# Kernel optimization log

Measured on AMD Instinct MI355X. Metric: run time of the kernel, lower is better.

The kernel has to match this reference:

```python
import jax, jax.numpy as jnp
import numpy as np

D_MODEL = 2048
NUM_Q_HEADS = 32
NUM_KV_HEADS = 8
HEAD_DIM = D_MODEL // NUM_Q_HEADS  # 64
NUM_GROUPS = NUM_Q_HEADS // NUM_KV_HEADS  # 4


def setup_inputs() -> dict:
    key = jax.random.key(0)
    ks = jax.random.split(key, 9)
    s = 1.0 / np.sqrt(D_MODEL)
    x = jax.random.normal(ks[0], (2, 2048, D_MODEL), dtype=jnp.float32)
    Wq = jax.random.uniform(ks[1], (D_MODEL, NUM_Q_HEADS * HEAD_DIM), jnp.float32, -s, s)
    bq = jax.random.uniform(ks[2], (NUM_Q_HEADS * HEAD_DIM,), jnp.float32, -s, s)
    Wk = jax.random.uniform(ks[3], (D_MODEL, NUM_KV_HEADS * HEAD_DIM), jnp.float32, -s, s)
    bk = jax.random.uniform(ks[4], (NUM_KV_HEADS * HEAD_DIM,), jnp.float32, -s, s)
    Wv = jax.random.uniform(ks[5], (D_MODEL, NUM_KV_HEADS * HEAD_DIM), jnp.float32, -s, s)
    bv = jax.random.uniform(ks[6], (NUM_KV_HEADS * HEAD_DIM,), jnp.float32, -s, s)
    Wo = jax.random.uniform(ks[7], (D_MODEL, D_MODEL), jnp.float32, -s, s)
    bo = jax.random.uniform(ks[8], (D_MODEL,), jnp.float32, -s, s)
    return {"x": x, "Wq": Wq, "bq": bq, "Wk": Wk, "bk": bk,
            "Wv": Wv, "bv": bv, "Wo": Wo, "bo": bo}


def reference(x, Wq, bq, Wk, bk, Wv, bv, Wo, bo):
    B, T, C = x.shape
    Hkv, G, Dh = NUM_KV_HEADS, NUM_GROUPS, HEAD_DIM
    # projections
    q = (x @ Wq + bq).reshape(B, T, Hkv, G, Dh)   # group G query heads per kv head
    k = (x @ Wk + bk).reshape(B, T, Hkv, Dh)
    v = (x @ Wv + bv).reshape(B, T, Hkv, Dh)
    scale = 1.0 / np.sqrt(Dh).astype(np.float32)
    # scores: [B, Hkv, G, T, T] (kv head broadcast over its G query heads)
    scores = jnp.einsum('btkgd,bskd->bkgts', q, k) * scale
    attn = jax.nn.softmax(scores, axis=-1)
    out = jnp.einsum('bkgts,bskd->btkgd', attn, v).reshape(B, T, C)
    return out @ Wo + bo
```

## Files before the change

kernel.cpp:

```cpp
#include <hip/hip_runtime.h>
#include <cstdint>
#include <cstddef>
#include <math.h>

typedef uint16_t bf16;
typedef __attribute__((ext_vector_type(8))) __bf16 bf16x8;
typedef __attribute__((ext_vector_type(4))) float f32x4;
typedef __attribute__((ext_vector_type(16))) float f32x16;

#define MFMA16(a,b,c) __builtin_amdgcn_mfma_f32_16x16x32_bf16((a),(b),(c),0,0,0)
#define MFMA32(a,b,c) __builtin_amdgcn_mfma_f32_32x32x16_bf16((a),(b),(c),0,0,0)

__device__ __forceinline__ uint16_t f2bf(float f){
  uint32_t u = __float_as_uint(f);
  return (uint16_t)((u + 0x7fffu + ((u >> 16) & 1u)) >> 16);
}
__device__ __forceinline__ uint32_t pk2(float lo, float hi){
  return (uint32_t)f2bf(lo) | ((uint32_t)f2bf(hi) << 16);
}

__device__ __forceinline__ void gload_lds16(const void* g, void* l){
  __builtin_amdgcn_global_load_lds((const __attribute__((address_space(1))) void*)g,
                                   (__attribute__((address_space(3))) void*)l, 16, 0, 0);
}

__device__ __forceinline__ void transpose64(const float* __restrict__ in, bf16* __restrict__ out,
                                            int R, int C, int c0, int r0, float* tileRaw){
  float (*tile)[65] = reinterpret_cast<float(*)[65]>(tileRaw);
  int t = threadIdx.x;
  int fx = t & 15, fy = t >> 4;
  #pragma unroll
  for (int i = 0; i < 4; i++){
    int r = fy + i*16;
    float4 v = *reinterpret_cast<const float4*>(in + (size_t)(r0 + r)*C + c0 + fx*4);
    tile[r][fx*4+0] = v.x; tile[r][fx*4+1] = v.y;
    tile[r][fx*4+2] = v.z; tile[r][fx*4+3] = v.w;
  }
  __syncthreads();
  int gx = t & 7, gy = t >> 3;
  #pragma unroll
  for (int i = 0; i < 2; i++){
    int c = gy + i*32;
    int rr = gx*8;
    union { bf16 h[8]; uint4 u; } pk_;
    #pragma unroll
    for (int j = 0; j < 8; j++) pk_.h[j] = f2bf(tile[rr+j][c]);
    *reinterpret_cast<uint4*>(out + (size_t)(c0 + c)*R + r0 + rr) = pk_.u;
  }
}

__global__ void k_prep(const float* __restrict__ x, bf16* __restrict__ xb,
                       const float* __restrict__ Wq, bf16* __restrict__ WqT,
                       const float* __restrict__ Wk, bf16* __restrict__ WkT,
                       const float* __restrict__ Wv, bf16* __restrict__ WvT,
                       const float* __restrict__ Wo, bf16* __restrict__ WoT,
                       const float* __restrict__ bq, const float* __restrict__ bk,
                       const float* __restrict__ bv, float* __restrict__ biasAll){
  __shared__ __align__(16) float tile[64*65];
  int b = blockIdx.x;
  if (b < 8192){
    int i = (b * 256 + threadIdx.x) * 4;
    float4 v = *reinterpret_cast<const float4*>(x + i);
    uint2 pkv = make_uint2(pk2(v.x, v.y), pk2(v.z, v.w));
    *reinterpret_cast<uint2*>(xb + i) = pkv;
  } else if (b < 9216){
    int idx = b - 8192;
    transpose64(Wq, WqT, 2048, 2048, (idx & 31)*64, (idx >> 5)*64, tile);
  } else if (b < 9472){
    int idx = b - 9216;
    transpose64(Wk, WkT, 2048, 512, (idx & 7)*64, (idx >> 3)*64, tile);
  } else if (b < 9728){
    int idx = b - 9472;
    transpose64(Wv, WvT, 2048, 512, (idx & 7)*64, (idx >> 3)*64, tile);
  } else if (b < 10752){
    int idx = b - 9728;
    transpose64(Wo, WoT, 2048, 2048, (idx & 31)*64, (idx >> 5)*64, tile);
  } else {
    int j = (b - 10752)*1024 + threadIdx.x*4;
    float4 v;
    if (j < 2048)      v = *reinterpret_cast<const float4*>(bq + j);
    else if (j < 2560) v = *reinterpret_cast<const float4*>(bk + j - 2048);
    else               v = *reinterpret_cast<const float4*>(bv + j - 2560);
    *reinterpret_cast<float4*>(biasAll + j) = v;
  }
}

__device__ __forceinline__ void gemm256x192_core(
    const bf16* __restrict__ Abase, const bf16* __restrict__ Btbase,
    char* lds, f32x4 acc[8][3])
{
  const int tid = threadIdx.x;
  const int wid = tid >> 6, lane = tid & 63;
  const int wm = wid >> 2, wn = wid & 3;
  const int lr = lane & 15, lg = lane >> 4;
  const f32x4 vzero = {0.f, 0.f, 0.f, 0.f};
  #pragma unroll
  for (int m = 0; m < 8; m++)
    #pragma unroll
    for (int n = 0; n < 3; n++)
      acc[m][n] = vzero;

  int srcA[4], srcB[3];
  #pragma unroll
  for (int i = 0; i < 4; i++){
    int db = i*8192 + tid*16;
    int row = db >> 7, sp = (db >> 4) & 7, sl = sp ^ (row & 7);
    srcA[i] = row*2048 + sl*8;
  }
  #pragma unroll
  for (int i = 0; i < 3; i++){
    int db = i*8192 + tid*16;
    int row = db >> 7, sp = (db >> 4) & 7, sl = sp ^ (row & 7);
    srcB[i] = row*2048 + sl*8;
  }
  const int dOf = wid*1024;

  int ksl[2];
  #pragma unroll
  for (int ks = 0; ks < 2; ks++) ksl[ks] = (((ks*4 + lg) ^ (lr & 7)) << 4);
  const int aB = wm*16384 + lr*128;
  const int bB = wn*6144 + lr*128;

  #define STG_A(bufOff, koff) do { \
    gload_lds16(Abase + (koff) + srcA[0], lds + (bufOff) + dOf); \
    gload_lds16(Abase + (koff) + srcA[1], lds + (bufOff) + 8192 + dOf); \
    gload_lds16(Abase + (koff) + srcA[2], lds + (bufOff) + 16384 + dOf); \
    gload_lds16(Abase + (koff) + srcA[3], lds + (bufOff) + 24576 + dOf); \
  } while(0)
  #define STG_B(bufOff, koff) do { \
    gload_lds16(Btbase + (koff) + srcB[0], lds + (bufOff) + dOf); \
    gload_lds16(Btbase + (koff) + srcB[1], lds + (bufOff) + 8192 + dOf); \
    gload_lds16(Btbase + (koff) + srcB[2], lds + (bufOff) + 16384 + dOf); \
  } while(0)

  STG_B(98304, 0);
  STG_A(0, 0);
  STG_A(32768, 64);
  asm volatile("s_waitcnt vmcnt(4)" ::: "memory");
  __builtin_amdgcn_s_barrier();

  bf16x8 afr[8], bfr[3];
  int aOff = 0;
  int bOff = 98304;
  for (int t = 0; t < 32; t++){
    const int aStg = (aOff == 0) ? 65536 : aOff - 32768;
    const int bNxt = bOff ^ 24576;

    #pragma unroll
    for (int am = 0; am < 8; am++)
      afr[am] = *reinterpret_cast<const bf16x8*>(lds + aOff + aB + am*2048 + ksl[0]);
    #pragma unroll
    for (int bn = 0; bn < 3; bn++)
      bfr[bn] = *reinterpret_cast<const bf16x8*>(lds + bOff + bB + bn*2048 + ksl[0]);
    if (t < 31) STG_B(bNxt, (t+1)*64);
    __builtin_amdgcn_s_barrier();
    asm volatile("s_waitcnt lgkmcnt(0)" ::: "memory");
    __builtin_amdgcn_sched_barrier(0);
    __builtin_amdgcn_s_setprio(1);
    #pragma unroll
    for (int am = 0; am < 8; am++)
      #pragma unroll
      for (int bn = 0; bn < 3; bn++)
        acc[am][bn] = MFMA16(afr[am], bfr[bn], acc[am][bn]);
    __builtin_amdgcn_s_setprio(0);
    __builtin_amdgcn_s_barrier();

    #pragma unroll
    for (int am = 0; am < 8; am++)
      afr[am] = *reinterpret_cast<const bf16x8*>(lds + aOff + aB + am*2048 + ksl[1]);
    #pragma unroll
    for (int bn = 0; bn < 3; bn++)
      bfr[bn] = *reinterpret_cast<const bf16x8*>(lds + bOff + bB + bn*2048 + ksl[1]);
    if (t < 30) STG_A(aStg, (t+2)*64);
    __builtin_amdgcn_s_barrier();
    asm volatile("s_waitcnt lgkmcnt(0)" ::: "memory");
    __builtin_amdgcn_sched_barrier(0);
    __builtin_amdgcn_s_setprio(1);
    #pragma unroll
    for (int am = 0; am < 8; am++)
      #pragma unroll
      for (int bn = 0; bn < 3; bn++)
        acc[am][bn] = MFMA16(afr[am], bfr[bn], acc[am][bn]);
    __builtin_amdgcn_s_setprio(0);
    if (t < 30)       asm volatile("s_waitcnt vmcnt(4)" ::: "memory");
    else if (t == 30) asm volatile("s_waitcnt vmcnt(0)" ::: "memory");
    __builtin_amdgcn_sched_barrier(0);
    __builtin_amdgcn_s_barrier();

    aOff = (aOff == 65536) ? 0 : aOff + 32768;
    bOff = bNxt;
  }
  #undef STG_A
  #undef STG_B
}

__device__ __forceinline__ void gemm256x128_core(
    const bf16* __restrict__ Abase, const bf16* __restrict__ Btbase,
    char* lds, f32x4 acc[4][4])
{
  const int tid = threadIdx.x;
  const int wid = tid >> 6, lane = tid & 63;
  const int wm = wid >> 1, wn = wid & 1;
  const int lr = lane & 15, lg = lane >> 4;
  const f32x4 vzero = {0.f, 0.f, 0.f, 0.f};
  #pragma unroll
  for (int m = 0; m < 4; m++)
    #pragma unroll
    for (int n = 0; n < 4; n++)
      acc[m][n] = vzero;

  int srcA[4], srcB[2];
  #pragma unroll
  for (int i = 0; i < 4; i++){
    int db = i*8192 + tid*16;
    int row = db >> 7, sp = (db >> 4) & 7, sl = sp ^ (row & 7);
    srcA[i] = row*2048 + sl*8;
  }
  #pragma unroll
  for (int i = 0; i < 2; i++){
    int db = i*8192 + tid*16;
    int row = db >> 7, sp = (db >> 4) & 7, sl = sp ^ (row & 7);
    srcB[i] = row*2048 + sl*8;
  }
  const int dOf = wid*1024;

  int ksl[2];
  #pragma unroll
  for (int ks = 0; ks < 2; ks++) ksl[ks] = (((ks*4 + lg) ^ (lr & 7)) << 4);
  const int aB = wm*8192 + lr*128;
  const int bB = wn*8192 + lr*128;

  #define STG_A(bufOff, koff) do { \
    gload_lds16(Abase + (koff) + srcA[0], lds + (bufOff) + dOf); \
    gload_lds16(Abase + (koff) + srcA[1], lds + (bufOff) + 8192 + dOf); \
    gload_lds16(Abase + (koff) + srcA[2], lds + (bufOff) + 16384 + dOf); \
    gload_lds16(Abase + (koff) + srcA[3], lds + (bufOff) + 24576 + dOf); \
  } while(0)
  #define STG_B(bufOff, koff) do { \
    gload_lds16(Btbase + (koff) + srcB[0], lds + (bufOff) + dOf); \
    gload_lds16(Btbase + (koff) + srcB[1], lds + (bufOff) + 8192 + dOf); \
  } while(0)

  STG_B(98304, 0);
  STG_A(0, 0);
  STG_B(114688, 64);
  STG_A(32768, 64);
  asm volatile("s_waitcnt vmcnt(6)" ::: "memory");
  __builtin_amdgcn_s_barrier();

  bf16x8 afr[4], bfr[4];
  int aOff = 0;
  int bIdx = 0;
  for (int t = 0; t < 32; t++){
    const int bOff = 98304 + bIdx*16384;
    const int aStg = (aOff == 0) ? 65536 : aOff - 32768;
    const int bStg = 98304 + ((bIdx == 0) ? 2 : bIdx - 1)*16384;

    #pragma unroll
    for (int am = 0; am < 4; am++)
      afr[am] = *reinterpret_cast<const bf16x8*>(lds + aOff + aB + am*2048 + ksl[0]);
    #pragma unroll
    for (int bn = 0; bn < 4; bn++)
      bfr[bn] = *reinterpret_cast<const bf16x8*>(lds + bOff + bB + bn*2048 + ksl[0]);
    if (t < 30) STG_B(bStg, (t+2)*64);
    __builtin_amdgcn_s_barrier();
    asm volatile("s_waitcnt lgkmcnt(0)" ::: "memory");
    __builtin_amdgcn_sched_barrier(0);
    __builtin_amdgcn_s_setprio(1);
    #pragma unroll
    for (int am = 0; am < 4; am++)
      #pragma unroll
      for (int bn = 0; bn < 4; bn++)
        acc[am][bn] = MFMA16(afr[am], bfr[bn], acc[am][bn]);
    __builtin_amdgcn_s_setprio(0);
    __builtin_amdgcn_s_barrier();

    #pragma unroll
    for (int am = 0; am < 4; am++)
      afr[am] = *reinterpret_cast<const bf16x8*>(lds + aOff + aB + am*2048 + ksl[1]);
    #pragma unroll
    for (int bn = 0; bn < 4; bn++)
      bfr[bn] = *reinterpret_cast<const bf16x8*>(lds + bOff + bB + bn*2048 + ksl[1]);
    if (t < 30) STG_A(aStg, (t+2)*64);
    __builtin_amdgcn_s_barrier();
    asm volatile("s_waitcnt lgkmcnt(0)" ::: "memory");
    __builtin_amdgcn_sched_barrier(0);
    __builtin_amdgcn_s_setprio(1);
    #pragma unroll
    for (int am = 0; am < 4; am++)
      #pragma unroll
      for (int bn = 0; bn < 4; bn++)
        acc[am][bn] = MFMA16(afr[am], bfr[bn], acc[am][bn]);
    __builtin_amdgcn_s_setprio(0);
    if (t < 30)       asm volatile("s_waitcnt vmcnt(6)" ::: "memory");
    else if (t == 30) asm volatile("s_waitcnt vmcnt(0)" ::: "memory");
    __builtin_amdgcn_sched_barrier(0);
    __builtin_amdgcn_s_barrier();

    aOff = (aOff == 65536) ? 0 : aOff + 32768;
    bIdx = (bIdx == 2) ? 0 : bIdx + 1;
  }
  #undef STG_A
  #undef STG_B
}

__global__ __launch_bounds__(512, 1) void k_qkv(
    const bf16* __restrict__ xb, const bf16* __restrict__ WT,
    const float* __restrict__ biasAll,
    bf16* __restrict__ qo, bf16* __restrict__ ko, bf16* __restrict__ vtp)
{
  __shared__ __align__(16) char lds[147456];
  int m0 = blockIdx.x * 256;
  int y  = blockIdx.y;
  f32x4 acc[8][3];
  gemm256x192_core(xb + (size_t)m0*2048, WT + (size_t)y*192*2048, lds, acc);
  const int tid = threadIdx.x, wid = tid >> 6, lane = tid & 63;
  const int wm = wid >> 2, wn = wid & 3, lr = lane & 15, lg = lane >> 4;
  #pragma unroll
  for (int bn = 0; bn < 3; bn++){
    int fb = y*192 + wn*48 + bn*16;
    float bb = biasAll[fb + lr];
    if (fb < 2048){
      #pragma unroll
      for (int am = 0; am < 8; am++)
        #pragma unroll
        for (int r = 0; r < 4; r++){
          int row = m0 + wm*128 + am*16 + lg*4 + r;
          qo[(size_t)row*2048 + fb + lr] = f2bf((acc[am][bn][r] + bb) * 0.18033688011112042f);
        }
    } else if (fb < 2560){
      int c = fb - 2048 + lr;
      #pragma unroll
      for (int am = 0; am < 8; am++)
        #pragma unroll
        for (int r = 0; r < 4; r++){
          int row = m0 + wm*128 + am*16 + lg*4 + r;
          ko[(size_t)row*512 + c] = f2bf(acc[am][bn][r] + bb);
        }
    } else {
      int vcol = fb - 2560 + lr;
      #pragma unroll
      for (int am = 0; am < 8; am++){
        int row0 = m0 + wm*128 + am*16 + lg*4;
        int bi = row0 >> 11, tl = row0 & 2047;
        union { bf16 h[4]; uint2 u; } pk_;
        #pragma unroll
        for (int r = 0; r < 4; r++) pk_.h[r] = f2bf(acc[am][bn][r] + bb);
        *reinterpret_cast<uint2*>(vtp + ((size_t)bi*512 + vcol)*2048 + tl) = pk_.u;
      }
    }
  }
}

__global__ __launch_bounds__(512, 1) void k_oproj(
    const bf16* __restrict__ ab, const bf16* __restrict__ WoT,
    const float* __restrict__ bo, float* __restrict__ outp)
{
  __shared__ __align__(16) char lds[147456];
  int m0 = blockIdx.x * 256, n0 = blockIdx.y * 128;
  f32x4 acc[4][4];
  gemm256x128_core(ab + (size_t)m0*2048, WoT + (size_t)n0*2048, lds, acc);
  const int tid = threadIdx.x, wid = tid >> 6, lane = tid & 63;
  const int wm = wid >> 1, wn = wid & 1, lr = lane & 15, lg = lane >> 4;
  #pragma unroll
  for (int bn = 0; bn < 4; bn++){
    int col = n0 + wn*64 + bn*16 + lr;
    float bb = bo[col];
    #pragma unroll
    for (int am = 0; am < 4; am++)
      #pragma unroll
      for (int r = 0; r < 4; r++){
        int row = m0 + wm*64 + am*16 + lg*4 + r;
        outp[(size_t)row*2048 + col] = acc[am][bn][r] + bb;
      }
  }
}

__global__ __launch_bounds__(512, 2) void k_flash(
    const bf16* __restrict__ q, const bf16* __restrict__ kmat,
    const bf16* __restrict__ vt, bf16* __restrict__ ao)
{
  __shared__ __align__(16) char lds[98304];
  const int tid = threadIdx.x;
  const int wid = tid >> 6, lane = tid & 63;
  const int l31 = lane & 31, hi = lane >> 5;
  const int bh = blockIdx.y;
  const int b = bh >> 5, hq = bh & 31, kvh = hq >> 2;
  const int qt = blockIdx.x;
  const int qrow0 = b*2048 + qt*512 + wid*64;

  bf16x8 qf[2][4];
  #pragma unroll
  for (int g = 0; g < 2; g++){
    const bf16* qrow = q + (size_t)(qrow0 + g*32 + l31)*2048 + hq*64 + hi*8;
    #pragma unroll
    for (int t = 0; t < 4; t++)
      qf[g][t] = *reinterpret_cast<const bf16x8*>(qrow + t*16);
  }

  f32x16 oacc[2][2];
  #pragma unroll
  for (int g = 0; g < 2; g++)
    #pragma unroll
    for (int n = 0; n < 2; n++)
      #pragma unroll
      for (int r = 0; r < 16; r++) oacc[g][n][r] = 0.f;
  float rsg[2][2];
  rsg[0][0]=0.f; rsg[0][1]=0.f; rsg[1][0]=0.f; rsg[1][1]=0.f;
  const f32x16 zv = {0.f,0.f,0.f,0.f,0.f,0.f,0.f,0.f,0.f,0.f,0.f,0.f,0.f,0.f,0.f,0.f};

  const int r7 = l31 & 7;
  int A[4];
  #pragma unroll
  for (int j = 0; j < 4; j++)
    A[j] = l31*128 + (((2*j + hi) ^ r7) << 4);

  const bf16* kbase = kmat + (size_t)b*2048*512 + kvh*64;
  const bf16* vbase = vt + ((size_t)b*512 + kvh*64)*2048;

  int kSrc[2], vSrc[2];
  const int dOf = wid*1024;
  #pragma unroll
  for (int i = 0; i < 2; i++){
    int kdb = i*8192 + tid*16;
    int krow = kdb >> 7, ksp = (kdb >> 4) & 7, ksl = ksp ^ (krow & 7);
    kSrc[i] = krow*512 + ksl*8;
    int o = tid*16;
    int vrow = o >> 7, vsp = (o >> 4) & 7, vsl = vsp ^ (vrow & 7);
    vSrc[i] = vrow*2048 + i*64 + vsl*8;
  }

  #define STAGE(bo, st_) do { \
    const bf16* kb_ = kbase + (size_t)(st_)*128*512; \
    const bf16* vb_ = vbase + (st_)*128; \
    gload_lds16(kb_ + kSrc[0], lds + (bo) + dOf); \
    gload_lds16(kb_ + kSrc[1], lds + (bo) + 8192 + dOf); \
    gload_lds16(vb_ + vSrc[0], lds + 49152 + (bo) + dOf); \
    gload_lds16(vb_ + vSrc[1], lds + 49152 + (bo) + 8192 + dOf); \
  } while(0)

  #define LDK(j, imm) (*reinterpret_cast<const bf16x8*>(lds + kOff + A[j] + (imm)))
  #define LDV(j, imm) (*reinterpret_cast<const bf16x8*>(lds + 49152 + kOff + A[j] + (imm)))

  STAGE(0, 0);
  STAGE(16384, 1);

  int kOff = 0;
  int sOff = 32768;
  for (int st = 0; st < 16; st++){
    if (st == 15) asm volatile("s_waitcnt vmcnt(0)" ::: "memory");
    else          asm volatile("s_waitcnt vmcnt(4)" ::: "memory");
    __builtin_amdgcn_sched_barrier(0);
    __builtin_amdgcn_s_barrier();
    __builtin_amdgcn_sched_barrier(0);
    if (st < 14){
      STAGE(sOff, st+2);
      sOff = (sOff == 32768) ? 0 : sOff + 16384;
    }

    #pragma unroll
    for (int c = 0; c < 2; c++){
      f32x16 sc[2][2];
      __builtin_amdgcn_s_setprio(1);
      #pragma unroll
      for (int t = 0; t < 4; t++){
        bf16x8 af0 = LDK(t, c*8192);
        bf16x8 af1 = LDK(t, c*8192 + 4096);
        if (t == 0){
          sc[0][0] = MFMA32(af0, qf[0][0], zv);
          sc[1][0] = MFMA32(af0, qf[1][0], zv);
          sc[0][1] = MFMA32(af1, qf[0][0], zv);
          sc[1][1] = MFMA32(af1, qf[1][0], zv);
        } else {
          sc[0][0] = MFMA32(af0, qf[0][t], sc[0][0]);
          sc[1][0] = MFMA32(af0, qf[1][t], sc[1][0]);
          sc[0][1] = MFMA32(af1, qf[0][t], sc[0][1]);
          sc[1][1] = MFMA32(af1, qf[1][t], sc[1][1]);
        }
      }
      __builtin_amdgcn_s_setprio(0);

      uint32_t pw[2][2][8];
      #pragma unroll
      for (int g = 0; g < 2; g++){
        #pragma unroll
        for (int n = 0; n < 2; n++)
          #pragma unroll
          for (int j = 0; j < 8; j++){
            float plo = __builtin_amdgcn_exp2f(sc[g][n][2*j]);
            float phi = __builtin_amdgcn_exp2f(sc[g][n][2*j+1]);
            rsg[g][j & 1] += plo + phi;
            asm("v_cvt_pk_bf16_f32 %0, %1, %2" : "=v"(pw[g][n][j]) : "v"(plo), "v"(phi));
          }
        #pragma unroll
        for (int n = 0; n < 2; n++)
          #pragma unroll
          for (int h = 0; h < 2; h++){
            asm volatile("v_permlane32_swap_b32 %0, %1" : "+v"(pw[g][n][h*4+0]), "+v"(pw[g][n][h*4+2]));
            asm volatile("v_permlane32_swap_b32 %0, %1" : "+v"(pw[g][n][h*4+1]), "+v"(pw[g][n][h*4+3]));
          }
      }

      __builtin_amdgcn_s_setprio(1);
      #pragma unroll
      for (int kk = 0; kk < 4; kk++){
        int n = kk >> 1, h = kk & 1;
        union { uint32_t w[4]; bf16x8 v; } pa0, pa1;
        #pragma unroll
        for (int w_ = 0; w_ < 4; w_++){ pa0.w[w_] = pw[0][n][h*4+w_]; pa1.w[w_] = pw[1][n][h*4+w_]; }
        #pragma unroll
        for (int nd = 0; nd < 2; nd++){
          bf16x8 vf = LDV(kk, c*8192 + nd*4096);
          oacc[0][nd] = MFMA32(pa0.v, vf, oacc[0][nd]);
          oacc[1][nd] = MFMA32(pa1.v, vf, oacc[1][nd]);
        }
      }
      __builtin_amdgcn_s_setprio(0);
    }
    kOff = (kOff == 32768) ? 0 : kOff + 16384;
  }
  #undef STAGE
  #undef LDK
  #undef LDV

  #pragma unroll
  for (int g = 0; g < 2; g++){
    float rs = rsg[g][0] + rsg[g][1];
    float l = rs + __shfl_xor(rs, 32);
    float linv = 1.f / l;
    float lv[16];
    #pragma unroll
    for (int r = 0; r < 16; r++){
      int qi = (r & 3) + 8*(r >> 2) + 4*hi;
      lv[r] = __shfl(linv, qi);
    }
    #pragma unroll
    for (int nd = 0; nd < 2; nd++)
      #pragma unroll
      for (int r = 0; r < 16; r++){
        int qi = (r & 3) + 8*(r >> 2) + 4*hi;
        int row = qrow0 + g*32 + qi;
        ao[(size_t)row*2048 + hq*64 + nd*32 + l31] = f2bf(oacc[g][nd][r] * lv[r]);
      }
  }
}

extern "C" void kernel_launch(void* const* d_in, const int* in_sizes, int n_in,
                              void* d_out, int out_size, void* d_ws, size_t ws_size,
                              hipStream_t stream)
{
  const float* x  = (const float*)d_in[0];
  const float* Wq = (const float*)d_in[1];
  const float* bq = (const float*)d_in[2];
  const float* Wk = (const float*)d_in[3];
  const float* bk = (const float*)d_in[4];
  const float* Wv = (const float*)d_in[5];
  const float* bv = (const float*)d_in[6];
  const float* Wo = (const float*)d_in[7];
  const float* bo = (const float*)d_in[8];
  float* out = (float*)d_out;

  char* ws = (char*)d_ws;
  size_t off = 0;
  auto alloc = [&](size_t bytes){ char* p = ws + off; off += (bytes + 255) & ~(size_t)255; return p; };
  bf16* xb  = (bf16*)alloc(2*2048*2048*2);
  bf16* WqT = (bf16*)alloc(2048*2048*2);
  bf16* WkT = (bf16*)alloc(512*2048*2);
  bf16* WvT = (bf16*)alloc(512*2048*2);
  bf16* WoT = (bf16*)alloc(2048*2048*2);
  bf16* qb  = (bf16*)alloc(4096*2048*2);
  bf16* kb  = (bf16*)alloc((size_t)4096*512*2);
  bf16* vtb = (bf16*)alloc((size_t)4096*512*2);
  float* biasAll = (float*)alloc(3072*4);
  bf16* aob = xb;

  k_prep<<<10755, 256, 0, stream>>>(x, xb, Wq, WqT, Wk, WkT, Wv, WvT, Wo, WoT, bq, bk, bv, biasAll);
  k_qkv<<<dim3(16,16), 512, 0, stream>>>(xb, WqT, biasAll, qb, kb, vtb);
  k_flash<<<dim3(4,64), 512, 0, stream>>>(qb, kb, vtb, aob);
  k_oproj<<<dim3(16,16), 512, 0, stream>>>(aob, WoT, bo, out);
}
```

Before: 181.7 us.

## Merge two k-halves per GEMM iteration and drop intra-iteration barriers

Both GEMM cores now issue all next-stage global->LDS prefetches at the top of each k-iteration. They then load both k-slices of A/B fragments from LDS at once and run all MFMAs in one block. The two mid-iteration barriers, the explicit lgkmcnt waits and the sched_barriers are removed, leaving one barrier per iteration and letting the compiler interleave LDS reads with MFMAs. This doubles the fragment registers held live, which raises register pressure. It also gives up the hand-controlled ordering of loads against MFMAs.

New measurement: 179.1 us, median of 2. Within noise of the previous version (-1.4%).

```diff
diff --git a/kernel.cpp b/kernel.cpp
--- a/kernel.cpp
+++ b/kernel.cpp
@@ -139,52 +139,39 @@
   asm volatile("s_waitcnt vmcnt(4)" ::: "memory");
   __builtin_amdgcn_s_barrier();
 
-  bf16x8 afr[8], bfr[3];
   int aOff = 0;
   int bOff = 98304;
   for (int t = 0; t < 32; t++){
     const int aStg = (aOff == 0) ? 65536 : aOff - 32768;
     const int bNxt = bOff ^ 24576;
 
+    if (t < 31) STG_B(bNxt, (t+1)*64);
+    if (t < 30) STG_A(aStg, (t+2)*64);
+
+    bf16x8 afr[8][2], bfr[3][2];
     #pragma unroll
     for (int am = 0; am < 8; am++)
-      afr[am] = *reinterpret_cast<const bf16x8*>(lds + aOff + aB + am*2048 + ksl[0]);
+      #pragma unroll
+      for (int ks = 0; ks < 2; ks++)
+        afr[am][ks] = *reinterpret_cast<const bf16x8*>(lds + aOff + aB + am*2048 + ksl[ks]);
     #pragma unroll
     for (int bn = 0; bn < 3; bn++)
-      bfr[bn] = *reinterpret_cast<const bf16x8*>(lds + bOff + bB + bn*2048 + ksl[0]);
-    if (t < 31) STG_B(bNxt, (t+1)*64);
-    __builtin_amdgcn_s_barrier();
-    asm volatile("s_waitcnt lgkmcnt(0)" ::: "memory");
-    __builtin_amdgcn_sched_barrier(0);
+      #pragma unroll
+      for (int ks = 0; ks < 2; ks++)
+        bfr[bn][ks] = *reinterpret_cast<const bf16x8*>(lds + bOff + bB + bn*2048 + ksl[ks]);
+
     __builtin_amdgcn_s_setprio(1);
     #pragma unroll
     for (int am = 0; am < 8; am++)
       #pragma unroll
       for (int bn = 0; bn < 3; bn++)
-        acc[am][bn] = MFMA16(afr[am], bfr[bn], acc[am][bn]);
+        #pragma unroll
+        for (int ks = 0; ks < 2; ks++)
+          acc[am][bn] = MFMA16(afr[am][ks], bfr[bn][ks], acc[am][bn]);
     __builtin_amdgcn_s_setprio(0);
-    __builtin_amdgcn_s_barrier();
-
-    #pragma unroll
-    for (int am = 0; am < 8; am++)
-      afr[am] = *reinterpret_cast<const bf16x8*>(lds + aOff + aB + am*2048 + ksl[1]);
-    #pragma unroll
-    for (int bn = 0; bn < 3; bn++)
-      bfr[bn] = *reinterpret_cast<const bf16x8*>(lds + bOff + bB + bn*2048 + ksl[1]);
-    if (t < 30) STG_A(aStg, (t+2)*64);
-    __builtin_amdgcn_s_barrier();
-    asm volatile("s_waitcnt lgkmcnt(0)" ::: "memory");
-    __builtin_amdgcn_sched_barrier(0);
-    __builtin_amdgcn_s_setprio(1);
-    #pragma unroll
-    for (int am = 0; am < 8; am++)
-      #pragma unroll
-      for (int bn = 0; bn < 3; bn++)
-        acc[am][bn] = MFMA16(afr[am], bfr[bn], acc[am][bn]);
-    __builtin_amdgcn_s_setprio(0);
+
     if (t < 30)       asm volatile("s_waitcnt vmcnt(4)" ::: "memory");
     else if (t == 30) asm volatile("s_waitcnt vmcnt(0)" ::: "memory");
-    __builtin_amdgcn_sched_barrier(0);
     __builtin_amdgcn_s_barrier();
 
     aOff = (aOff == 65536) ? 0 : aOff + 32768;
@@ -248,7 +235,6 @@
   asm volatile("s_waitcnt vmcnt(6)" ::: "memory");
   __builtin_amdgcn_s_barrier();
 
-  bf16x8 afr[4], bfr[4];
   int aOff = 0;
   int bIdx = 0;
   for (int t = 0; t < 32; t++){
@@ -256,45 +242,35 @@
     const int aStg = (aOff == 0) ? 65536 : aOff - 32768;
     const int bStg = 98304 + ((bIdx == 0) ? 2 : bIdx - 1)*16384;
 
+    if (t < 30){
+      STG_B(bStg, (t+2)*64);
+      STG_A(aStg, (t+2)*64);
+    }
+
+    bf16x8 afr[4][2], bfr[4][2];
     #pragma unroll
     for (int am = 0; am < 4; am++)
-      afr[am] = *reinterpret_cast<const bf16x8*>(lds + aOff + aB + am*2048 + ksl[0]);
+      #pragma unroll
+      for (int ks = 0; ks < 2; ks++)
+        afr[am][ks] = *reinterpret_cast<const bf16x8*>(lds + aOff + aB + am*2048 + ksl[ks]);
     #pragma unroll
     for (int bn = 0; bn < 4; bn++)
-      bfr[bn] = *reinterpret_cast<const bf16x8*>(lds + bOff + bB + bn*2048 + ksl[0]);
-    if (t < 30) STG_B(bStg, (t+2)*64);
-    __builtin_amdgcn_s_barrier();
-    asm volatile("s_waitcnt lgkmcnt(0)" ::: "memory");
-    __builtin_amdgcn_sched_barrier(0);
+      #pragma unroll
+      for (int ks = 0; ks < 2; ks++)
+        bfr[bn][ks] = *reinterpret_cast<const bf16x8*>(lds + bOff + bB + bn*2048 + ksl[ks]);
+
     __builtin_amdgcn_s_setprio(1);
     #pragma unroll
     for (int am = 0; am < 4; am++)
       #pragma unroll
       for (int bn = 0; bn < 4; bn++)
-        acc[am][bn] = MFMA16(afr[am], bfr[bn], acc[am][bn]);
+        #pragma unroll
+        for (int ks = 0; ks < 2; ks++)
+          acc[am][bn] = MFMA16(afr[am][ks], bfr[bn][ks], acc[am][bn]);
     __builtin_amdgcn_s_setprio(0);
-    __builtin_amdgcn_s_barrier();
-
-    #pragma unroll
-    for (int am = 0; am < 4; am++)
-      afr[am] = *reinterpret_cast<const bf16x8*>(lds + aOff + aB + am*2048 + ksl[1]);
-    #pragma unroll
-    for (int bn = 0; bn < 4; bn++)
-      bfr[bn] = *reinterpret_cast<const bf16x8*>(lds + bOff + bB + bn*2048 + ksl[1]);
-    if (t < 30) STG_A(aStg, (t+2)*64);
-    __builtin_amdgcn_s_barrier();
-    asm volatile("s_waitcnt lgkmcnt(0)" ::: "memory");
-    __builtin_amdgcn_sched_barrier(0);
-    __builtin_amdgcn_s_setprio(1);
-    #pragma unroll
-    for (int am = 0; am < 4; am++)
-      #pragma unroll
-      for (int bn = 0; bn < 4; bn++)
-        acc[am][bn] = MFMA16(afr[am], bfr[bn], acc[am][bn]);
-    __builtin_amdgcn_s_setprio(0);
+
     if (t < 30)       asm volatile("s_waitcnt vmcnt(6)" ::: "memory");
     else if (t == 30) asm volatile("s_waitcnt vmcnt(0)" ::: "memory");
-    __builtin_amdgcn_sched_barrier(0);
     __builtin_amdgcn_s_barrier();
 
     aOff = (aOff == 65536) ? 0 : aOff + 32768;
```
